# Kernel optimization log

Hardware: AMD Instinct MI355X
Metric: run time of the kernel (lower is better)

Reference implementation:

```python
import jax, jax.numpy as jnp
import numpy as np

EPS = 1e-6
WEIGHT_THRESHOLD = 0.0


def setup_inputs() -> dict:
    key = jax.random.key(0)
    kA, kB, kW = jax.random.split(key, 3)
    bs, n = 200000, 20
    A = jax.random.normal(kA, (bs, n, 3), dtype=jnp.float32)
    B = jax.random.normal(kB, (bs, n, 3), dtype=jnp.float32)
    weights = jax.random.uniform(kW, (bs, n), dtype=jnp.float32)
    return {"A": A, "B": B, "weights": weights}


def reference(A, B, weights):
    """Batched weighted Procrustes (Kabsch). A,B: [bs,n,3], weights: [bs,n].
    Returns SE3 transforms [bs,4,4], matching rigid_transform_3d + integrate_trans."""
    w = jnp.where(weights < WEIGHT_THRESHOLD, 0.0, weights)
    wsum = jnp.sum(w, axis=1, keepdims=True)[:, :, None] + EPS  # [bs,1,1]
    centroid_A = jnp.sum(A * w[:, :, None], axis=1, keepdims=True) / wsum  # [bs,1,3]
    centroid_B = jnp.sum(B * w[:, :, None], axis=1, keepdims=True) / wsum
    Am = A - centroid_A
    Bm = B - centroid_B
    # H = Am^T diag(w) Bm  -> [bs,3,3]
    H = jnp.einsum('bni,bn,bnj->bij', Am, w, Bm)
    U, S, Vh = jnp.linalg.svd(H)          # H = U S Vh
    V = jnp.swapaxes(Vh, -1, -2)          # torch.svd's "Vt" is actually V
    Ut = jnp.swapaxes(U, -1, -2)
    delta = jnp.linalg.det(V @ Ut)        # [bs]
    corr = jnp.broadcast_to(jnp.eye(3, dtype=A.dtype), V.shape).copy()
    corr = corr.at[:, 2, 2].set(delta)
    R = V @ corr @ Ut                     # [bs,3,3]
    t = jnp.swapaxes(centroid_B, 1, 2) - R @ jnp.swapaxes(centroid_A, 1, 2)  # [bs,3,1]
    top = jnp.concatenate([R, t], axis=-1)  # [bs,3,4]
    bottom = jnp.broadcast_to(jnp.array([0.0, 0.0, 0.0, 1.0], dtype=A.dtype), (A.shape[0], 1, 4))
    return jnp.concatenate([top, bottom], axis=1)  # [bs,4,4]
```

## Files before the change

### kernel.cpp

```cpp
#include <hip/hip_runtime.h>

#define EPS_W 1e-6f

__device__ __forceinline__ float fast_rsq(float x) { return __builtin_amdgcn_rsqf(x); }
__device__ __forceinline__ float fast_rcp(float x) { return __builtin_amdgcn_rcpf(x); }

__device__ __forceinline__ void solve16(const float S[16], float R[9], float t[3])
{
    const float sw  = S[0];
    const float Sa0 = S[1], Sa1 = S[2], Sa2 = S[3];
    const float Sb0 = S[4], Sb1 = S[5], Sb2 = S[6];

    const float inv = fast_rcp(sw + EPS_W);
    const float cA0 = Sa0*inv, cA1 = Sa1*inv, cA2 = Sa2*inv;
    const float cB0 = Sb0*inv, cB1 = Sb1*inv, cB2 = Sb2*inv;

    float H[3][3];
    H[0][0] = S[7]  - cA0*Sb0 - Sa0*cB0 + sw*cA0*cB0;
    H[0][1] = S[8]  - cA0*Sb1 - Sa0*cB1 + sw*cA0*cB1;
    H[0][2] = S[9]  - cA0*Sb2 - Sa0*cB2 + sw*cA0*cB2;
    H[1][0] = S[10] - cA1*Sb0 - Sa1*cB0 + sw*cA1*cB0;
    H[1][1] = S[11] - cA1*Sb1 - Sa1*cB1 + sw*cA1*cB1;
    H[1][2] = S[12] - cA1*Sb2 - Sa1*cB2 + sw*cA1*cB2;
    H[2][0] = S[13] - cA2*Sb0 - Sa2*cB0 + sw*cA2*cB0;
    H[2][1] = S[14] - cA2*Sb1 - Sa2*cB1 + sw*cA2*cB1;
    H[2][2] = S[15] - cA2*Sb2 - Sa2*cB2 + sw*cA2*cB2;

    const float Sxx=H[0][0], Sxy=H[0][1], Sxz=H[0][2];
    const float Syx=H[1][0], Syy=H[1][1], Syz=H[1][2];
    const float Szx=H[2][0], Szy=H[2][1], Szz=H[2][2];

    float Nm[4][4];
    Nm[0][0] =  Sxx+Syy+Szz; Nm[0][1] = Syz-Szy;      Nm[0][2] = Szx-Sxz;      Nm[0][3] = Sxy-Syx;
    Nm[1][0] =  Nm[0][1];    Nm[1][1] = Sxx-Syy-Szz;  Nm[1][2] = Sxy+Syx;      Nm[1][3] = Szx+Sxz;
    Nm[2][0] =  Nm[0][2];    Nm[2][1] = Nm[1][2];     Nm[2][2] = -Sxx+Syy-Szz; Nm[2][3] = Syz+Szy;
    Nm[3][0] =  Nm[0][3];    Nm[3][1] = Nm[1][3];     Nm[3][2] = Nm[2][3];     Nm[3][3] = -Sxx-Syy+Szz;

    float Vv[4][4] = {{1.f,0.f,0.f,0.f},{0.f,1.f,0.f,0.f},{0.f,0.f,1.f,0.f},{0.f,0.f,0.f,1.f}};

    for (int sweep = 0; sweep < 5; ++sweep) {
        #pragma unroll
        for (int pair = 0; pair < 6; ++pair) {
            constexpr int PP[6] = {0,0,0,1,1,2};
            constexpr int QQ[6] = {1,2,3,2,3,3};
            const int p = PP[pair], q = QQ[pair];
            float d  = Nm[p][p] - Nm[q][q];
            float o  = Nm[p][q];
            float r2 = d*d + 4.f*o*o;
            bool tiny = r2 < 1e-30f;
            float rinv = fast_rsq(tiny ? 1.f : r2);
            float hh = 0.5f + 0.5f * fabsf(d) * rinv;
            float ci = fast_rsq(hh);
            float c  = hh * ci;
            float s  = (d < 0.f ? o : -o) * rinv * ci;
            c = tiny ? 1.f : c;
            s = tiny ? 0.f : s;
            #pragma unroll
            for (int k = 0; k < 4; ++k) {
                float akp = Nm[k][p], akq = Nm[k][q];
                Nm[k][p] = c*akp - s*akq;
                Nm[k][q] = s*akp + c*akq;
            }
            #pragma unroll
            for (int k = 0; k < 4; ++k) {
                float apk = Nm[p][k], aqk = Nm[q][k];
                Nm[p][k] = c*apk - s*aqk;
                Nm[q][k] = s*apk + c*aqk;
            }
            #pragma unroll
            for (int k = 0; k < 4; ++k) {
                float vkp = Vv[k][p], vkq = Vv[k][q];
                Vv[k][p] = c*vkp - s*vkq;
                Vv[k][q] = s*vkp + c*vkq;
            }
        }
    }

    float q0=Vv[0][0], q1=Vv[1][0], q2=Vv[2][0], q3=Vv[3][0];
    float best = Nm[0][0];
    #pragma unroll
    for (int m = 1; m < 4; ++m) {
        bool bt = Nm[m][m] > best;
        best = bt ? Nm[m][m] : best;
        q0 = bt ? Vv[0][m] : q0;
        q1 = bt ? Vv[1][m] : q1;
        q2 = bt ? Vv[2][m] : q2;
        q3 = bt ? Vv[3][m] : q3;
    }
    float qn = fast_rsq(q0*q0 + q1*q1 + q2*q2 + q3*q3);
    q0*=qn; q1*=qn; q2*=qn; q3*=qn;

    float R00 = q0*q0+q1*q1-q2*q2-q3*q3;
    float R01 = 2.f*(q1*q2 - q0*q3);
    float R02 = 2.f*(q1*q3 + q0*q2);
    float R10 = 2.f*(q1*q2 + q0*q3);
    float R11 = q0*q0-q1*q1+q2*q2-q3*q3;
    float R12 = 2.f*(q2*q3 - q0*q1);
    float R20 = 2.f*(q1*q3 - q0*q2);
    float R21 = 2.f*(q2*q3 + q0*q1);
    float R22 = q0*q0-q1*q1-q2*q2+q3*q3;

    float trRH  = R00*Sxx+R01*Syx+R02*Szx
                + R10*Sxy+R11*Syy+R12*Szy
                + R20*Sxz+R21*Syz+R22*Szz;
    float trRtH = R00*Sxx+R01*Sxy+R02*Sxz
                + R10*Syx+R11*Syy+R12*Syz
                + R20*Szx+R21*Szy+R22*Szz;
    if (trRtH > trRH) {
        float tt;
        tt = R01; R01 = R10; R10 = tt;
        tt = R02; R02 = R20; R20 = tt;
        tt = R12; R12 = R21; R21 = tt;
    }

    R[0]=R00; R[1]=R01; R[2]=R02;
    R[3]=R10; R[4]=R11; R[5]=R12;
    R[6]=R20; R[7]=R21; R[8]=R22;
    t[0] = cB0 - (R00*cA0 + R01*cA1 + R02*cA2);
    t[1] = cB1 - (R10*cA0 + R11*cA1 + R12*cA2);
    t[2] = cB2 - (R20*cA0 + R21*cA1 + R22*cA2);
}

__global__ __launch_bounds__(256) void kabsch_fused20_kernel(
    const float* __restrict__ A, const float* __restrict__ B,
    const float* __restrict__ W, float* __restrict__ Out, int bs)
{
    __shared__ float sums[128][17];

    const int tid = threadIdx.x;
    const int blk = blockIdx.x;
    const int il  = tid >> 1;
    const int h   = tid & 1;
    int item = blk * 128 + il;
    int itemc = item < bs ? item : (bs - 1);

    const float2* A2 = reinterpret_cast<const float2*>(A);
    const float2* B2 = reinterpret_cast<const float2*>(B);
    const float2* W2 = reinterpret_cast<const float2*>(W);
    const int abase = itemc*30 + h*15;
    const int wbase = itemc*10 + h*5;

    float sw = 0.f;
    float Sa0=0.f,Sa1=0.f,Sa2=0.f, Sb0=0.f,Sb1=0.f,Sb2=0.f;
    float M00=0.f,M01=0.f,M02=0.f,M10=0.f,M11=0.f,M12=0.f,M20=0.f,M21=0.f,M22=0.f;

    #pragma unroll
    for (int g = 0; g < 5; ++g) {
        float2 a0 = A2[abase+3*g+0], a1 = A2[abase+3*g+1], a2 = A2[abase+3*g+2];
        float2 b0 = B2[abase+3*g+0], b1 = B2[abase+3*g+1], b2 = B2[abase+3*g+2];
        float2 wv = W2[wbase+g];
        float w0 = wv.x < 0.f ? 0.f : wv.x;
        float w1 = wv.y < 0.f ? 0.f : wv.y;

        {
            float ax=a0.x, ay=a0.y, az=a1.x;
            float bx=b0.x, by=b0.y, bz=b1.x;
            sw += w0;
            float wax=w0*ax, way=w0*ay, waz=w0*az;
            Sa0+=wax; Sa1+=way; Sa2+=waz;
            Sb0+=w0*bx; Sb1+=w0*by; Sb2+=w0*bz;
            M00+=wax*bx; M01+=wax*by; M02+=wax*bz;
            M10+=way*bx; M11+=way*by; M12+=way*bz;
            M20+=waz*bx; M21+=waz*by; M22+=waz*bz;
        }
        {
            float ax=a1.y, ay=a2.x, az=a2.y;
            float bx=b1.y, by=b2.x, bz=b2.y;
            sw += w1;
            float wax=w1*ax, way=w1*ay, waz=w1*az;
            Sa0+=wax; Sa1+=way; Sa2+=waz;
            Sb0+=w1*bx; Sb1+=w1*by; Sb2+=w1*bz;
            M00+=wax*bx; M01+=wax*by; M02+=wax*bz;
            M10+=way*bx; M11+=way*by; M12+=way*bz;
            M20+=waz*bx; M21+=waz*by; M22+=waz*bz;
        }
    }

    sw  += __shfl_xor(sw, 1);
    Sa0 += __shfl_xor(Sa0,1); Sa1 += __shfl_xor(Sa1,1); Sa2 += __shfl_xor(Sa2,1);
    Sb0 += __shfl_xor(Sb0,1); Sb1 += __shfl_xor(Sb1,1); Sb2 += __shfl_xor(Sb2,1);
    M00 += __shfl_xor(M00,1); M01 += __shfl_xor(M01,1); M02 += __shfl_xor(M02,1);
    M10 += __shfl_xor(M10,1); M11 += __shfl_xor(M11,1); M12 += __shfl_xor(M12,1);
    M20 += __shfl_xor(M20,1); M21 += __shfl_xor(M21,1); M22 += __shfl_xor(M22,1);

    if (h == 0) {
        sums[il][0]=sw;
        sums[il][1]=Sa0;  sums[il][2]=Sa1;  sums[il][3]=Sa2;
        sums[il][4]=Sb0;  sums[il][5]=Sb1;  sums[il][6]=Sb2;
        sums[il][7]=M00;  sums[il][8]=M01;  sums[il][9]=M02;
        sums[il][10]=M10; sums[il][11]=M11; sums[il][12]=M12;
        sums[il][13]=M20; sums[il][14]=M21; sums[il][15]=M22;
    }
    __syncthreads();

    if (tid < 128) {
        const int item2 = blk * 128 + tid;
        if (item2 < bs) {
            float S[16];
            #pragma unroll
            for (int k = 0; k < 16; ++k) S[k] = sums[tid][k];
            float R[9], t[3];
            solve16(S, R, t);
            float4* O4 = reinterpret_cast<float4*>(Out + (size_t)item2 * 16);
            O4[0] = make_float4(R[0], R[1], R[2], t[0]);
            O4[1] = make_float4(R[3], R[4], R[5], t[1]);
            O4[2] = make_float4(R[6], R[7], R[8], t[2]);
            O4[3] = make_float4(0.f, 0.f, 0.f, 1.f);
        }
    }
}

__global__ __launch_bounds__(256) void kabsch_generic_kernel(
    const float* __restrict__ A, const float* __restrict__ B,
    const float* __restrict__ W, float* __restrict__ Out,
    int bs, int n)
{
    const int b = blockIdx.x * blockDim.x + threadIdx.x;
    if (b >= bs) return;

    float S[16];
    #pragma unroll
    for (int k = 0; k < 16; ++k) S[k] = 0.f;

    for (int j = 0; j < n; ++j) {
        const float* ap = A + ((size_t)b * n + j) * 3;
        const float* bp = B + ((size_t)b * n + j) * 3;
        float w = W[(size_t)b * n + j];
        w = w < 0.f ? 0.f : w;
        float ax=ap[0], ay=ap[1], az=ap[2];
        float bx=bp[0], by=bp[1], bz=bp[2];
        S[0] += w;
        float wax = w*ax, way = w*ay, waz = w*az;
        S[1] += wax; S[2] += way; S[3] += waz;
        S[4] += w*bx; S[5] += w*by; S[6] += w*bz;
        S[7] += wax*bx; S[8]  += wax*by; S[9]  += wax*bz;
        S[10]+= way*bx; S[11] += way*by; S[12] += way*bz;
        S[13]+= waz*bx; S[14] += waz*by; S[15] += waz*bz;
    }

    float R[9], t[3];
    solve16(S, R, t);

    float4* O4 = reinterpret_cast<float4*>(Out + (size_t)b * 16);
    O4[0] = make_float4(R[0], R[1], R[2], t[0]);
    O4[1] = make_float4(R[3], R[4], R[5], t[1]);
    O4[2] = make_float4(R[6], R[7], R[8], t[2]);
    O4[3] = make_float4(0.f, 0.f, 0.f, 1.f);
}

extern "C" void kernel_launch(void* const* d_in, const int* in_sizes, int n_in,
                              void* d_out, int out_size, void* d_ws, size_t ws_size,
                              hipStream_t stream) {
    const float* A = (const float*)d_in[0];
    const float* B = (const float*)d_in[1];
    const float* W = (const float*)d_in[2];
    float* Out = (float*)d_out;
    const int bs = out_size / 16;
    const int n  = (bs > 0) ? (in_sizes[2] / bs) : 0;
    if (n == 20) {
        const int blocks = (bs + 127) / 128;
        hipLaunchKernelGGL(kabsch_fused20_kernel, dim3(blocks), dim3(256), 0, stream,
                           A, B, W, Out, bs);
    } else {
        const int blocks = (bs + 255) / 256;
        hipLaunchKernelGGL(kabsch_generic_kernel, dim3(blocks), dim3(256), 0, stream,
                           A, B, W, Out, bs, n);
    }
}
```

Before: 146.4 us.

## Stage inputs through LDS with coalesced float4 loads, one thread per item

```diff
diff --git a/kernel.cpp b/kernel.cpp
--- a/kernel.cpp
+++ b/kernel.cpp
@@ -121,92 +121,90 @@
     t[2] = cB2 - (R20*cA0 + R21*cA1 + R22*cA2);
 }
 
-__global__ __launch_bounds__(256) void kabsch_fused20_kernel(
+#define ITEMS_PB 64
+
+__global__ __launch_bounds__(256) void kabsch_lds20_kernel(
     const float* __restrict__ A, const float* __restrict__ B,
     const float* __restrict__ W, float* __restrict__ Out, int bs)
 {
-    __shared__ float sums[128][17];
+    __shared__ float sA[ITEMS_PB * 61];
+    __shared__ float sB[ITEMS_PB * 61];
+    __shared__ float sW[ITEMS_PB * 21];
+    __shared__ float sO[ITEMS_PB * 17];
 
     const int tid = threadIdx.x;
     const int blk = blockIdx.x;
-    const int il  = tid >> 1;
-    const int h   = tid & 1;
-    int item = blk * 128 + il;
-    int itemc = item < bs ? item : (bs - 1);
-
-    const float2* A2 = reinterpret_cast<const float2*>(A);
-    const float2* B2 = reinterpret_cast<const float2*>(B);
-    const float2* W2 = reinterpret_cast<const float2*>(W);
-    const int abase = itemc*30 + h*15;
-    const int wbase = itemc*10 + h*5;
-
-    float sw = 0.f;
-    float Sa0=0.f,Sa1=0.f,Sa2=0.f, Sb0=0.f,Sb1=0.f,Sb2=0.f;
-    float M00=0.f,M01=0.f,M02=0.f,M10=0.f,M11=0.f,M12=0.f,M20=0.f,M21=0.f,M22=0.f;
-
-    #pragma unroll
-    for (int g = 0; g < 5; ++g) {
-        float2 a0 = A2[abase+3*g+0], a1 = A2[abase+3*g+1], a2 = A2[abase+3*g+2];
-        float2 b0 = B2[abase+3*g+0], b1 = B2[abase+3*g+1], b2 = B2[abase+3*g+2];
-        float2 wv = W2[wbase+g];
-        float w0 = wv.x < 0.f ? 0.f : wv.x;
-        float w1 = wv.y < 0.f ? 0.f : wv.y;
-
-        {
-            float ax=a0.x, ay=a0.y, az=a1.x;
-            float bx=b0.x, by=b0.y, bz=b1.x;
-            sw += w0;
-            float wax=w0*ax, way=w0*ay, waz=w0*az;
-            Sa0+=wax; Sa1+=way; Sa2+=waz;
-            Sb0+=w0*bx; Sb1+=w0*by; Sb2+=w0*bz;
-            M00+=wax*bx; M01+=wax*by; M02+=wax*bz;
-            M10+=way*bx; M11+=way*by; M12+=way*bz;
-            M20+=waz*bx; M21+=waz*by; M22+=waz*bz;
+    const int base_item = blk * ITEMS_PB;
+    int itemcnt = bs - base_item;
+    if (itemcnt > ITEMS_PB) itemcnt = ITEMS_PB;
+
+    const float4* Ag = reinterpret_cast<const float4*>(A) + (size_t)base_item * 15;
+    const float4* Bg = reinterpret_cast<const float4*>(B) + (size_t)base_item * 15;
+    const float4* Wg = reinterpret_cast<const float4*>(W) + (size_t)base_item * 5;
+
+    const int nf4 = itemcnt * 15;
+    for (int j = tid; j < nf4; j += 256) {
+        const int it = j / 15;
+        const int wi = j - it * 15;
+        float4 v = Ag[j];
+        float* d = &sA[it * 61 + wi * 4];
+        d[0] = v.x; d[1] = v.y; d[2] = v.z; d[3] = v.w;
+        float4 u = Bg[j];
+        float* e = &sB[it * 61 + wi * 4];
+        e[0] = u.x; e[1] = u.y; e[2] = u.z; e[3] = u.w;
+    }
+    const int nw4 = itemcnt * 5;
+    for (int j = tid; j < nw4; j += 256) {
+        const int it = j / 5;
+        const int wi = j - it * 5;
+        float4 v = Wg[j];
+        float* d = &sW[it * 21 + wi * 4];
+        d[0] = v.x; d[1] = v.y; d[2] = v.z; d[3] = v.w;
+    }
+    __syncthreads();
+
+    if (tid < itemcnt) {
+        const float* a = &sA[tid * 61];
+        const float* b = &sB[tid * 61];
+        const float* w = &sW[tid * 21];
+
+        float S[16];
+        #pragma unroll
+        for (int k = 0; k < 16; ++k) S[k] = 0.f;
+
+        #pragma unroll
+        for (int p = 0; p < 20; ++p) {
+            float wv = w[p];
+            wv = wv < 0.f ? 0.f : wv;
+            float ax = a[3*p+0], ay = a[3*p+1], az = a[3*p+2];
+            float bx = b[3*p+0], by = b[3*p+1], bz = b[3*p+2];
+            S[0] += wv;
+            float wax = wv*ax, way = wv*ay, waz = wv*az;
+            S[1] += wax; S[2] += way; S[3] += waz;
+            S[4] += wv*bx; S[5] += wv*by; S[6] += wv*bz;
+            S[7]  += wax*bx; S[8]  += wax*by; S[9]  += wax*bz;
+            S[10] += way*bx; S[11] += way*by; S[12] += way*bz;
+            S[13] += waz*bx; S[14] += waz*by; S[15] += waz*bz;
         }
-        {
-            float ax=a1.y, ay=a2.x, az=a2.y;
-            float bx=b1.y, by=b2.x, bz=b2.y;
-            sw += w1;
-            float wax=w1*ax, way=w1*ay, waz=w1*az;
-            Sa0+=wax; Sa1+=way; Sa2+=waz;
-            Sb0+=w1*bx; Sb1+=w1*by; Sb2+=w1*bz;
-            M00+=wax*bx; M01+=wax*by; M02+=wax*bz;
-            M10+=way*bx; M11+=way*by; M12+=way*bz;
-            M20+=waz*bx; M21+=waz*by; M22+=waz*bz;
-        }
-    }
-
-    sw  += __shfl_xor(sw, 1);
-    Sa0 += __shfl_xor(Sa0,1); Sa1 += __shfl_xor(Sa1,1); Sa2 += __shfl_xor(Sa2,1);
-    Sb0 += __shfl_xor(Sb0,1); Sb1 += __shfl_xor(Sb1,1); Sb2 += __shfl_xor(Sb2,1);
-    M00 += __shfl_xor(M00,1); M01 += __shfl_xor(M01,1); M02 += __shfl_xor(M02,1);
-    M10 += __shfl_xor(M10,1); M11 += __shfl_xor(M11,1); M12 += __shfl_xor(M12,1);
-    M20 += __shfl_xor(M20,1); M21 += __shfl_xor(M21,1); M22 += __shfl_xor(M22,1);
-
-    if (h == 0) {
-        sums[il][0]=sw;
-        sums[il][1]=Sa0;  sums[il][2]=Sa1;  sums[il][3]=Sa2;
-        sums[il][4]=Sb0;  sums[il][5]=Sb1;  sums[il][6]=Sb2;
-        sums[il][7]=M00;  sums[il][8]=M01;  sums[il][9]=M02;
-        sums[il][10]=M10; sums[il][11]=M11; sums[il][12]=M12;
-        sums[il][13]=M20; sums[il][14]=M21; sums[il][15]=M22;
+
+        float R[9], t[3];
+        solve16(S, R, t);
+
+        float* o = &sO[tid * 17];
+        o[0]=R[0];  o[1]=R[1];  o[2]=R[2];  o[3]=t[0];
+        o[4]=R[3];  o[5]=R[4];  o[6]=R[5];  o[7]=t[1];
+        o[8]=R[6];  o[9]=R[7];  o[10]=R[8]; o[11]=t[2];
+        o[12]=0.f;  o[13]=0.f;  o[14]=0.f;  o[15]=1.f;
     }
     __syncthreads();
 
-    if (tid < 128) {
-        const int item2 = blk * 128 + tid;
-        if (item2 < bs) {
-            float S[16];
-            #pragma unroll
-            for (int k = 0; k < 16; ++k) S[k] = sums[tid][k];
-            float R[9], t[3];
-            solve16(S, R, t);
-            float4* O4 = reinterpret_cast<float4*>(Out + (size_t)item2 * 16);
-            O4[0] = make_float4(R[0], R[1], R[2], t[0]);
-            O4[1] = make_float4(R[3], R[4], R[5], t[1]);
-            O4[2] = make_float4(R[6], R[7], R[8], t[2]);
-            O4[3] = make_float4(0.f, 0.f, 0.f, 1.f);
-        }
+    const int no4 = itemcnt * 4;
+    float4* Og = reinterpret_cast<float4*>(Out) + (size_t)base_item * 4;
+    for (int j = tid; j < no4; j += 256) {
+        const int it = j >> 2;
+        const int wi = j & 3;
+        const float* o = &sO[it * 17 + wi * 4];
+        Og[j] = make_float4(o[0], o[1], o[2], o[3]);
     }
 }
 
@@ -258,8 +256,8 @@
     const int bs = out_size / 16;
     const int n  = (bs > 0) ? (in_sizes[2] / bs) : 0;
     if (n == 20) {
-        const int blocks = (bs + 127) / 128;
-        hipLaunchKernelGGL(kabsch_fused20_kernel, dim3(blocks), dim3(256), 0, stream,
+        const int blocks = (bs + ITEMS_PB - 1) / ITEMS_PB;
+        hipLaunchKernelGGL(kabsch_lds20_kernel, dim3(blocks), dim3(256), 0, stream,
                            A, B, W, Out, bs);
     } else {
         const int blocks = (bs + 255) / 256;
```

Result: slower. 166.3 us (+13.6%).

## Stage A, B, W through LDS with coalesced float4 loads and XOR swizzle

Applied to the files above, without the earlier changes.

```diff
diff --git a/kernel.cpp b/kernel.cpp
--- a/kernel.cpp
+++ b/kernel.cpp
@@ -1,6 +1,7 @@
 #include <hip/hip_runtime.h>
 
 #define EPS_W 1e-6f
+#define IPB 128
 
 __device__ __forceinline__ float fast_rsq(float x) { return __builtin_amdgcn_rsqf(x); }
 __device__ __forceinline__ float fast_rcp(float x) { return __builtin_amdgcn_rcpf(x); }
@@ -121,92 +122,130 @@
     t[2] = cB2 - (R20*cA0 + R21*cA1 + R22*cA2);
 }
 
-__global__ __launch_bounds__(256) void kabsch_fused20_kernel(
+__global__ __launch_bounds__(256, 4) void kabsch_swz20_kernel(
     const float* __restrict__ A, const float* __restrict__ B,
     const float* __restrict__ W, float* __restrict__ Out, int bs)
 {
-    __shared__ float sums[128][17];
-
-    const int tid = threadIdx.x;
-    const int blk = blockIdx.x;
-    const int il  = tid >> 1;
-    const int h   = tid & 1;
-    int item = blk * 128 + il;
-    int itemc = item < bs ? item : (bs - 1);
-
-    const float2* A2 = reinterpret_cast<const float2*>(A);
-    const float2* B2 = reinterpret_cast<const float2*>(B);
-    const float2* W2 = reinterpret_cast<const float2*>(W);
-    const int abase = itemc*30 + h*15;
-    const int wbase = itemc*10 + h*5;
-
-    float sw = 0.f;
-    float Sa0=0.f,Sa1=0.f,Sa2=0.f, Sb0=0.f,Sb1=0.f,Sb2=0.f;
-    float M00=0.f,M01=0.f,M02=0.f,M10=0.f,M11=0.f,M12=0.f,M20=0.f,M21=0.f,M22=0.f;
-
+    __shared__ float sbuf[8192];
+    float4* s4 = reinterpret_cast<float4*>(sbuf);
+    float2* s2 = reinterpret_cast<float2*>(sbuf);
+
+    const int tid  = threadIdx.x;
+    const int base = blockIdx.x * IPB;
+    int itemcnt = bs - base;
+    if (itemcnt > IPB) itemcnt = IPB;
+
+    const int i = tid >> 1;
+    const int h = tid & 1;
+    const bool act = (i < itemcnt);
+
+    const float4* Wg = reinterpret_cast<const float4*>(W) + (size_t)base * 5;
+    const int nW4 = itemcnt * 5;
+    for (int g = tid; g < nW4; g += 256) {
+        const int it = g / 5, c = g - it * 5;
+        s4[it * 6 + c] = Wg[g];
+    }
+    __syncthreads();
+    float wv[10];
+    if (act) {
+        #pragma unroll
+        for (int g = 0; g < 5; ++g) {
+            float2 v = s2[i * 12 + 5 * h + g];
+            wv[2*g] = v.x; wv[2*g+1] = v.y;
+        }
+    }
+    __syncthreads();
+
+    const float4* Ag = reinterpret_cast<const float4*>(A) + (size_t)base * 15;
+    const int n4 = itemcnt * 15;
+    for (int g = tid; g < n4; g += 256) {
+        const int it = g / 15, c = g - it * 15;
+        s4[(it << 4) + (c ^ (it & 15))] = Ag[g];
+    }
+    __syncthreads();
+    float2 av[15];
+    if (act) {
+        #pragma unroll
+        for (int j = 0; j < 15; ++j) {
+            const int s = 15 * h + j;
+            const int c = s >> 1, r = s & 1;
+            av[j] = s2[(i << 5) + (((c ^ (i & 15)) << 1) | r)];
+        }
+    }
+    __syncthreads();
+
+    const float4* Bg = reinterpret_cast<const float4*>(B) + (size_t)base * 15;
+    for (int g = tid; g < n4; g += 256) {
+        const int it = g / 15, c = g - it * 15;
+        s4[(it << 4) + (c ^ (it & 15))] = Bg[g];
+    }
+    __syncthreads();
+    float2 bv[15];
+    if (act) {
+        #pragma unroll
+        for (int j = 0; j < 15; ++j) {
+            const int s = 15 * h + j;
+            const int c = s >> 1, r = s & 1;
+            bv[j] = s2[(i << 5) + (((c ^ (i & 15)) << 1) | r)];
+        }
+    }
+
+    float S[16];
     #pragma unroll
-    for (int g = 0; g < 5; ++g) {
-        float2 a0 = A2[abase+3*g+0], a1 = A2[abase+3*g+1], a2 = A2[abase+3*g+2];
-        float2 b0 = B2[abase+3*g+0], b1 = B2[abase+3*g+1], b2 = B2[abase+3*g+2];
-        float2 wv = W2[wbase+g];
-        float w0 = wv.x < 0.f ? 0.f : wv.x;
-        float w1 = wv.y < 0.f ? 0.f : wv.y;
-
-        {
-            float ax=a0.x, ay=a0.y, az=a1.x;
-            float bx=b0.x, by=b0.y, bz=b1.x;
-            sw += w0;
-            float wax=w0*ax, way=w0*ay, waz=w0*az;
-            Sa0+=wax; Sa1+=way; Sa2+=waz;
-            Sb0+=w0*bx; Sb1+=w0*by; Sb2+=w0*bz;
-            M00+=wax*bx; M01+=wax*by; M02+=wax*bz;
-            M10+=way*bx; M11+=way*by; M12+=way*bz;
-            M20+=waz*bx; M21+=waz*by; M22+=waz*bz;
-        }
-        {
-            float ax=a1.y, ay=a2.x, az=a2.y;
-            float bx=b1.y, by=b2.x, bz=b2.y;
-            sw += w1;
-            float wax=w1*ax, way=w1*ay, waz=w1*az;
-            Sa0+=wax; Sa1+=way; Sa2+=waz;
-            Sb0+=w1*bx; Sb1+=w1*by; Sb2+=w1*bz;
-            M00+=wax*bx; M01+=wax*by; M02+=wax*bz;
-            M10+=way*bx; M11+=way*by; M12+=way*bz;
-            M20+=waz*bx; M21+=waz*by; M22+=waz*bz;
-        }
-    }
-
-    sw  += __shfl_xor(sw, 1);
-    Sa0 += __shfl_xor(Sa0,1); Sa1 += __shfl_xor(Sa1,1); Sa2 += __shfl_xor(Sa2,1);
-    Sb0 += __shfl_xor(Sb0,1); Sb1 += __shfl_xor(Sb1,1); Sb2 += __shfl_xor(Sb2,1);
-    M00 += __shfl_xor(M00,1); M01 += __shfl_xor(M01,1); M02 += __shfl_xor(M02,1);
-    M10 += __shfl_xor(M10,1); M11 += __shfl_xor(M11,1); M12 += __shfl_xor(M12,1);
-    M20 += __shfl_xor(M20,1); M21 += __shfl_xor(M21,1); M22 += __shfl_xor(M22,1);
-
-    if (h == 0) {
-        sums[il][0]=sw;
-        sums[il][1]=Sa0;  sums[il][2]=Sa1;  sums[il][3]=Sa2;
-        sums[il][4]=Sb0;  sums[il][5]=Sb1;  sums[il][6]=Sb2;
-        sums[il][7]=M00;  sums[il][8]=M01;  sums[il][9]=M02;
-        sums[il][10]=M10; sums[il][11]=M11; sums[il][12]=M12;
-        sums[il][13]=M20; sums[il][14]=M21; sums[il][15]=M22;
-    }
-    __syncthreads();
-
-    if (tid < 128) {
-        const int item2 = blk * 128 + tid;
-        if (item2 < bs) {
-            float S[16];
-            #pragma unroll
-            for (int k = 0; k < 16; ++k) S[k] = sums[tid][k];
-            float R[9], t[3];
-            solve16(S, R, t);
-            float4* O4 = reinterpret_cast<float4*>(Out + (size_t)item2 * 16);
-            O4[0] = make_float4(R[0], R[1], R[2], t[0]);
-            O4[1] = make_float4(R[3], R[4], R[5], t[1]);
-            O4[2] = make_float4(R[6], R[7], R[8], t[2]);
-            O4[3] = make_float4(0.f, 0.f, 0.f, 1.f);
-        }
+    for (int k = 0; k < 16; ++k) S[k] = 0.f;
+    if (act) {
+        #pragma unroll
+        for (int g = 0; g < 5; ++g) {
+            float2 a0 = av[3*g+0], a1 = av[3*g+1], a2 = av[3*g+2];
+            float2 b0 = bv[3*g+0], b1 = bv[3*g+1], b2 = bv[3*g+2];
+            float w0 = wv[2*g]   < 0.f ? 0.f : wv[2*g];
+            float w1 = wv[2*g+1] < 0.f ? 0.f : wv[2*g+1];
+            {
+                float ax=a0.x, ay=a0.y, az=a1.x;
+                float bx=b0.x, by=b0.y, bz=b1.x;
+                S[0] += w0;
+                float wax=w0*ax, way=w0*ay, waz=w0*az;
+                S[1]+=wax; S[2]+=way; S[3]+=waz;
+                S[4]+=w0*bx; S[5]+=w0*by; S[6]+=w0*bz;
+                S[7] +=wax*bx; S[8] +=wax*by; S[9] +=wax*bz;
+                S[10]+=way*bx; S[11]+=way*by; S[12]+=way*bz;
+                S[13]+=waz*bx; S[14]+=waz*by; S[15]+=waz*bz;
+            }
+            {
+                float ax=a1.y, ay=a2.x, az=a2.y;
+                float bx=b1.y, by=b2.x, bz=b2.y;
+                S[0] += w1;
+                float wax=w1*ax, way=w1*ay, waz=w1*az;
+                S[1]+=wax; S[2]+=way; S[3]+=waz;
+                S[4]+=w1*bx; S[5]+=w1*by; S[6]+=w1*bz;
+                S[7] +=wax*bx; S[8] +=wax*by; S[9] +=wax*bz;
+                S[10]+=way*bx; S[11]+=way*by; S[12]+=way*bz;
+                S[13]+=waz*bx; S[14]+=waz*by; S[15]+=waz*bz;
+            }
+        }
+    }
+
+    #pragma unroll
+    for (int k = 0; k < 16; ++k) S[k] += __shfl_xor(S[k], 1);
+
+    __syncthreads();
+    if (h == 0 && act) {
+        #pragma unroll
+        for (int k = 0; k < 16; ++k) sbuf[17 * i + k] = S[k];
+    }
+    __syncthreads();
+
+    if (tid < itemcnt) {
+        float Ss[16];
+        #pragma unroll
+        for (int k = 0; k < 16; ++k) Ss[k] = sbuf[17 * tid + k];
+        float R[9], t[3];
+        solve16(Ss, R, t);
+        float4* O4 = reinterpret_cast<float4*>(Out + (size_t)(base + tid) * 16);
+        O4[0] = make_float4(R[0], R[1], R[2], t[0]);
+        O4[1] = make_float4(R[3], R[4], R[5], t[1]);
+        O4[2] = make_float4(R[6], R[7], R[8], t[2]);
+        O4[3] = make_float4(0.f, 0.f, 0.f, 1.f);
     }
 }
 
@@ -258,8 +297,8 @@
     const int bs = out_size / 16;
     const int n  = (bs > 0) ? (in_sizes[2] / bs) : 0;
     if (n == 20) {
-        const int blocks = (bs + 127) / 128;
-        hipLaunchKernelGGL(kabsch_fused20_kernel, dim3(blocks), dim3(256), 0, stream,
+        const int blocks = (bs + IPB - 1) / IPB;
+        hipLaunchKernelGGL(kabsch_swz20_kernel, dim3(blocks), dim3(256), 0, stream,
                            A, B, W, Out, bs);
     } else {
         const int blocks = (bs + 255) / 256;
```

After: 166.9 us. 14.0% more time.
